# Performance work log

Hardware: AMD Instinct MI355X
Metric: run time of the kernel (lower is better)

Reference implementation:

```python
import jax, jax.numpy as jnp
import numpy as np

D_MODEL = 1024
NUM_HEADS = 16
HEAD_DIM = D_MODEL // NUM_HEADS
SEQ_LEN = 2048
THETA = 10000.0


def setup_inputs() -> dict:
    key = jax.random.key(0)
    ks = jax.random.split(key, 9)
    s = 1.0 / np.sqrt(D_MODEL)
    inp = {
        "x": jax.random.normal(ks[0], (2, SEQ_LEN, D_MODEL), dtype=jnp.float32),
        "Wq": jax.random.uniform(ks[1], (D_MODEL, D_MODEL), jnp.float32, -s, s),
        "bq": jax.random.uniform(ks[2], (D_MODEL,), jnp.float32, -s, s),
        "Wk": jax.random.uniform(ks[3], (D_MODEL, D_MODEL), jnp.float32, -s, s),
        "bk": jax.random.uniform(ks[4], (D_MODEL,), jnp.float32, -s, s),
        "Wv": jax.random.uniform(ks[5], (D_MODEL, D_MODEL), jnp.float32, -s, s),
        "bv": jax.random.uniform(ks[6], (D_MODEL,), jnp.float32, -s, s),
        "Wo": jax.random.uniform(ks[7], (D_MODEL, D_MODEL), jnp.float32, -s, s),
        "bo": jax.random.uniform(ks[8], (D_MODEL,), jnp.float32, -s, s),
    }
    return inp


def _rope_cos_sin(seq_len, dim, theta):
    inv_freq = 1.0 / theta ** (jnp.arange(0, dim, 2, dtype=jnp.float32) / dim)  # [dim/2]
    t = jnp.arange(seq_len, dtype=jnp.float32)
    freqs = jnp.outer(t, inv_freq)  # [S, dim/2]
    return jnp.cos(freqs), jnp.sin(freqs)


def _apply_rope(x, cos, sin):
    # x: [B, H, S, head_dim]; interleaved complex pairs (even, odd)
    x2 = x.reshape(*x.shape[:-1], -1, 2)  # [B,H,S,hd/2,2]
    xe, xo = x2[..., 0], x2[..., 1]
    c = cos[None, None, :, :]
    s = sin[None, None, :, :]
    oe = xe * c - xo * s
    oo = xe * s + xo * c
    return jnp.stack([oe, oo], axis=-1).reshape(x.shape)


def reference(x, Wq, bq, Wk, bk, Wv, bv, Wo, bo):
    B, S, D = x.shape
    H, hd = NUM_HEADS, HEAD_DIM
    q = x @ Wq.T + bq
    k = x @ Wk.T + bk
    v = x @ Wv.T + bv
    # [B, H, S, hd]
    q = q.reshape(B, S, H, hd).transpose(0, 2, 1, 3)
    k = k.reshape(B, S, H, hd).transpose(0, 2, 1, 3)
    v = v.reshape(B, S, H, hd).transpose(0, 2, 1, 3)
    cos, sin = _rope_cos_sin(S, hd, THETA)
    q = _apply_rope(q, cos, sin)
    k = _apply_rope(k, cos, sin)
    scores = jnp.einsum("bhqd,bhkd->bhqk", q, k) / jnp.sqrt(jnp.float32(hd))
    causal = jnp.triu(jnp.ones((S, S), dtype=bool), k=1)
    scores = jnp.where(causal[None, None, :, :], -jnp.inf, scores)
    attn = jax.nn.softmax(scores, axis=-1)
    out = jnp.einsum("bhqk,bhkd->bhqd", attn, v)
    out = out.transpose(0, 2, 1, 3).reshape(B, S, D)
    return out @ Wo.T + bo
```

## Files before the change

### kernel.cpp

```cpp
#include <hip/hip_runtime.h>
#include <hip/hip_bf16.h>

#define S_LEN 2048
#define DM 1024
#define NH 16
#define HD 64
#define M_ROWS 4096
#define LOG2E 1.4426950408889634f
#define MASKVAL -1.0e4f
#define QSCALE 0.18033688011112042f

typedef __attribute__((ext_vector_type(8))) short short8;
typedef __attribute__((ext_vector_type(2))) float f32x2;
typedef __attribute__((ext_vector_type(4))) float f32x4;
typedef __attribute__((ext_vector_type(16))) float f32x16;

__device__ inline ushort f2b(float f) {
  union { float f; unsigned u; } v; v.f = f;
  unsigned r = v.u + 0x7fffu + ((v.u >> 16) & 1u);
  return (ushort)(r >> 16);
}

__device__ inline float b2f(ushort u) {
  union { unsigned u; float f; } v; v.u = ((unsigned)u) << 16; return v.f;
}

__device__ inline unsigned pk_bf16(float a, float b) {
  __hip_bfloat162 h = __float22bfloat162_rn(make_float2(a, b));
  union { __hip_bfloat162 h; unsigned u; } v; v.h = h;
  return v.u;
}

__device__ inline float fexp2(float x) { return __builtin_amdgcn_exp2f(x); }

__device__ inline void gl_lds16(const void* g, void* l) {
  __builtin_amdgcn_global_load_lds(
      (const __attribute__((address_space(1))) void*)g,
      (__attribute__((address_space(3))) void*)l, 16, 0, 0);
}

__global__ __launch_bounds__(256) void cast_rope_kernel(
    const float* __restrict__ x, const float* __restrict__ Wq, const float* __restrict__ Wk,
    const float* __restrict__ Wv, const float* __restrict__ Wo,
    ushort* __restrict__ xb, ushort* __restrict__ Wqb, ushort* __restrict__ Wkb,
    ushort* __restrict__ Wvb, ushort* __restrict__ Wob,
    float* __restrict__ ropeC, float* __restrict__ ropeS) {
  const int bid = blockIdx.x;
  if (bid >= 8192) {
    int idx = (bid - 8192) * 256 + threadIdx.x;
    int s = idx >> 5, i = idx & 31;
    float inv = exp2f(-(float)i * (13.287712379549449f / 32.0f));
    float a = (float)s * inv;
    ropeC[idx] = cosf(a);
    ropeS[idx] = sinf(a);
    return;
  }
  int i = bid * 256 + threadIdx.x;
  int r = i >> 18, off = i & 0x3FFFF;
  const float4* s;
  uint2* d;
  switch (r) {
    case 0: case 1: case 2: case 3: s = (const float4*)x + i;  d = (uint2*)xb + i;  break;
    case 4: s = (const float4*)Wq + off; d = (uint2*)Wqb + off; break;
    case 5: s = (const float4*)Wk + off; d = (uint2*)Wkb + off; break;
    case 6: s = (const float4*)Wv + off; d = (uint2*)Wvb + off; break;
    default: s = (const float4*)Wo + off; d = (uint2*)Wob + off; break;
  }
  float4 v = *s;
  uint2 o;
  o.x = pk_bf16(v.x, v.y);
  o.y = pk_bf16(v.z, v.w);
  *d = o;
}

__global__ __launch_bounds__(256) void gemm_qkv_kernel(const ushort* __restrict__ xb,
    const ushort* __restrict__ Wqb, const ushort* __restrict__ Wkb, const ushort* __restrict__ Wvb,
    const float* __restrict__ bq, const float* __restrict__ bk, const float* __restrict__ bv,
    const float* __restrict__ ropeC, const float* __restrict__ ropeS,
    ushort* __restrict__ qb, ushort* __restrict__ kb, ushort* __restrict__ vT) {
  __shared__ ushort lds[24576];
  const int lid = blockIdx.x;
  const int swz = (lid & 7) * 96 + (lid >> 3);
  const int z = swz >> 8;
  const int rem = swz & 255;
  const int m0 = (rem & 31) * 128, n0 = (rem >> 5) * 128;
  const ushort* W = (z == 0) ? Wqb : ((z == 1) ? Wkb : Wvb);
  const float* bias = (z == 0) ? bq : ((z == 1) ? bk : bv);
  const int t = threadIdx.x, lane = t & 63, wave = t >> 6;
  const int wr = (wave >> 1) * 64, wc = (wave & 1) * 64;
  const int lr = lane & 15, lg = lane >> 4;

  const int slot0 = wave * 128 + lane, slot1 = slot0 + 64;
  const int row0 = slot0 >> 2, g0 = (slot0 & 3) ^ (row0 & 3);
  const int row1 = slot1 >> 2, g1 = (slot1 & 3) ^ (row1 & 3);
  const ushort* Ap0 = &xb[(size_t)(m0 + row0) * DM + g0 * 8];
  const ushort* Ap1 = &xb[(size_t)(m0 + row1) * DM + g1 * 8];
  const ushort* Wp0 = &W[(size_t)(n0 + row0) * DM + g0 * 8];
  const ushort* Wp1 = &W[(size_t)(n0 + row1) * DM + g1 * 8];

  f32x4 acc[4][4];
#pragma unroll
  for (int a = 0; a < 4; a++)
#pragma unroll
    for (int b = 0; b < 4; b++) acc[a][b] = (f32x4){0.f, 0.f, 0.f, 0.f};

  gl_lds16(Ap0, &lds[slot0 * 8]);
  gl_lds16(Ap1, &lds[slot1 * 8]);
  gl_lds16(Wp0, &lds[12288 + slot0 * 8]);
  gl_lds16(Wp1, &lds[12288 + slot1 * 8]);
  gl_lds16(Ap0 + 32, &lds[4096 + slot0 * 8]);
  gl_lds16(Ap1 + 32, &lds[4096 + slot1 * 8]);
  gl_lds16(Wp0 + 32, &lds[16384 + slot0 * 8]);
  gl_lds16(Wp1 + 32, &lds[16384 + slot1 * 8]);
  asm volatile("s_waitcnt vmcnt(4)" ::: "memory");
  __builtin_amdgcn_s_barrier();
  __builtin_amdgcn_sched_barrier(0);

  int cur = 0;
  for (int i = 0; i < 32; i++) {
    const bool pref = (i + 2 < 32);
    if (pref) {
      const int nb = (cur >= 1) ? cur - 1 : 2;
      const int k0 = (i + 2) * 32;
      gl_lds16(Ap0 + k0, &lds[nb * 4096 + slot0 * 8]);
      gl_lds16(Ap1 + k0, &lds[nb * 4096 + slot1 * 8]);
      gl_lds16(Wp0 + k0, &lds[12288 + nb * 4096 + slot0 * 8]);
      gl_lds16(Wp1 + k0, &lds[12288 + nb * 4096 + slot1 * 8]);
    }
    const int fb = cur * 4096;
    short8 af[4], bf[4];
#pragma unroll
    for (int mt = 0; mt < 4; mt++) {
      const int row = wr + mt * 16 + lr;
      af[mt] = *(const short8*)&lds[fb + (row * 4 + (lg ^ (row & 3))) * 8];
    }
#pragma unroll
    for (int nt = 0; nt < 4; nt++) {
      const int row = wc + nt * 16 + lr;
      bf[nt] = *(const short8*)&lds[12288 + fb + (row * 4 + (lg ^ (row & 3))) * 8];
    }
#pragma unroll
    for (int mt = 0; mt < 4; mt++)
#pragma unroll
      for (int nt = 0; nt < 4; nt++)
        acc[mt][nt] = __builtin_amdgcn_mfma_f32_16x16x32_bf16(af[mt], bf[nt], acc[mt][nt], 0, 0, 0);
    if (i + 1 < 32) {
      if (pref) asm volatile("s_waitcnt vmcnt(4)" ::: "memory");
      else      asm volatile("s_waitcnt vmcnt(0)" ::: "memory");
      __builtin_amdgcn_s_barrier();
      __builtin_amdgcn_sched_barrier(0);
    }
    cur = (cur >= 2) ? 0 : cur + 1;
  }
  __syncthreads();

#pragma unroll
  for (int mt = 0; mt < 4; mt++) {
#pragma unroll
    for (int nt = 0; nt < 4; nt++) {
      const int nloc = wc + nt * 16 + lr;
      const float bn = bias[n0 + nloc];
#pragma unroll
      for (int r = 0; r < 4; r++) {
        const int mloc = wr + mt * 16 + lg * 4 + r;
        const ushort v = f2b(acc[mt][nt][r] + bn);
        if (z < 2) lds[mloc * 136 + nloc] = v;
        else       lds[nloc * 136 + mloc] = v;
      }
    }
  }
  __syncthreads();

  const int b = m0 >> 11;
  if (z < 2) {
    ushort* dst = (z == 0) ? qb : kb;
    const float qscale = (z == 0) ? QSCALE : 1.0f;
#pragma unroll
    for (int c = 0; c < 8; c++) {
      const int sloc = c * 16 + (t >> 4);
      const int nloc = (t & 15) * 8;
      short8 val = *(const short8*)&lds[sloc * 136 + nloc];
      const int s = (m0 + sloc) & (S_LEN - 1);
      const int h = (n0 + nloc) >> 6;
      const int d0 = nloc & 63;
      const float4 cv = *(const float4*)&ropeC[s * 32 + d0 / 2];
      const float4 sv = *(const float4*)&ropeS[s * 32 + d0 / 2];
      uint4 o;
      {
        float e = b2f((ushort)val[0]), od = b2f((ushort)val[1]);
        o.x = pk_bf16((e * cv.x - od * sv.x) * qscale, (e * sv.x + od * cv.x) * qscale);
      }
      {
        float e = b2f((ushort)val[2]), od = b2f((ushort)val[3]);
        o.y = pk_bf16((e * cv.y - od * sv.y) * qscale, (e * sv.y + od * cv.y) * qscale);
      }
      {
        float e = b2f((ushort)val[4]), od = b2f((ushort)val[5]);
        o.z = pk_bf16((e * cv.z - od * sv.z) * qscale, (e * sv.z + od * cv.z) * qscale);
      }
      {
        float e = b2f((ushort)val[6]), od = b2f((ushort)val[7]);
        o.w = pk_bf16((e * cv.w - od * sv.w) * qscale, (e * sv.w + od * cv.w) * qscale);
      }
      *(uint4*)&dst[(((size_t)b * NH + h) * S_LEN + s) * HD + d0] = o;
    }
  } else {
    const int sbase = m0 & (S_LEN - 1);
#pragma unroll
    for (int c = 0; c < 8; c++) {
      const int nloc = c * 16 + (t >> 4);
      const int s0 = (t & 15) * 8;
      short8 val = *(const short8*)&lds[nloc * 136 + s0];
      const int h = (n0 + nloc) >> 6;
      const int d = nloc & 63;
      *(short8*)&vT[(((size_t)b * NH + h) * HD + d) * S_LEN + sbase + s0] = val;
    }
  }
}

__global__ __launch_bounds__(256) void flash_kernel(const ushort* __restrict__ qb,
                                                    const ushort* __restrict__ kb,
                                                    const ushort* __restrict__ vT,
                                                    ushort* __restrict__ attn) {
  __shared__ ushort lds[24576];
  const int t = threadIdx.x, lane = t & 63, wave = t >> 6;
  const int q31 = lane & 31, h = lane >> 5;
  const int lid = blockIdx.x;
  const int g = lid >> 5;
  const int qt = (g < 8) ? (15 - g) : (g - 8);
  const int bh = lid & 31;
  const int q0 = qt * 128;
  const int ntiles = 2 * qt + 2;
  const int kstart = 0;
  const int kend = ntiles;

  const ushort* kbh = kb + (size_t)bh * S_LEN * HD;
  const ushort* vbh = vT + (size_t)bh * HD * S_LEN;

  const int qrow = q0 + wave * 32 + q31;
  const ushort* qptr = qb + ((size_t)bh * S_LEN + qrow) * HD + h * 8;
  short8 qf[4];
#pragma unroll
  for (int s = 0; s < 4; s++) qf[s] = *(const short8*)(qptr + s * 16);

  const int slot0 = wave * 128 + lane, slot1 = slot0 + 64;
  const int row0 = slot0 >> 3, g0 = (slot0 & 7) ^ (row0 & 7);
  const int row1 = slot1 >> 3, g1 = (slot1 & 7) ^ (row1 & 7);
  const int lo0 = wave * 128 * 8, lo1 = lo0 + 64 * 8;

  int foff[4][2];
#pragma unroll
  for (int s = 0; s < 4; s++)
#pragma unroll
    for (int st = 0; st < 2; st++) {
      const int row = st * 32 + q31;
      foff[s][st] = (row * 8 + ((2 * s + h) ^ (row & 7))) * 8;
    }

  const ushort* kp0 = kbh + (size_t)row0 * HD + g0 * 8;
  const ushort* kp1 = kbh + (size_t)row1 * HD + g1 * 8;
  const ushort* vp0 = vbh + (size_t)row0 * S_LEN + g0 * 8;
  const ushort* vp1 = vbh + (size_t)row1 * S_LEN + g1 * 8;
  gl_lds16(kp0, &lds[lo0]);
  gl_lds16(kp1, &lds[lo1]);
  gl_lds16(vp0, &lds[12288 + lo0]);
  gl_lds16(vp1, &lds[12288 + lo1]);
  kp0 += 64 * HD; kp1 += 64 * HD; vp0 += 64; vp1 += 64;
  gl_lds16(kp0, &lds[4096 + lo0]);
  gl_lds16(kp1, &lds[4096 + lo1]);
  gl_lds16(vp0, &lds[16384 + lo0]);
  gl_lds16(vp1, &lds[16384 + lo1]);
  kp0 += 64 * HD; kp1 += 64 * HD; vp0 += 64; vp1 += 64;

  f32x16 O[2];
#pragma unroll
  for (int st = 0; st < 2; st++)
#pragma unroll
    for (int r = 0; r < 16; r++) O[st][r] = 0.f;

  f32x16 zc;
#pragma unroll
  for (int r = 0; r < 16; r++) zc[r] = 0.f;

  f32x2 lpA = (f32x2){0.f, 0.f}, lpB = (f32x2){0.f, 0.f};

  asm volatile("s_waitcnt vmcnt(4)" ::: "memory");
  __builtin_amdgcn_s_barrier();
  __builtin_amdgcn_sched_barrier(0);

  int cur = 0;
  for (int kt = kstart; kt < kend; ++kt) {
    const bool pref = (kt + 2 < kend);
    if (pref) {
      const int nb = (cur >= 1) ? cur - 1 : 2;
      const int ko = nb * 4096, vo = 12288 + nb * 4096;
      gl_lds16(kp0, &lds[ko + lo0]);
      gl_lds16(kp1, &lds[ko + lo1]);
      gl_lds16(vp0, &lds[vo + lo0]);
      gl_lds16(vp1, &lds[vo + lo1]);
      kp0 += 64 * HD; kp1 += 64 * HD; vp0 += 64; vp1 += 64;
    }
    const ushort* Kb = &lds[cur * 4096];
    const ushort* Vb = &lds[12288 + cur * 4096];

    f32x16 sc0, sc1;
    __builtin_amdgcn_s_setprio(1);
    sc0 = __builtin_amdgcn_mfma_f32_32x32x16_bf16(
        *(const short8*)&Kb[foff[0][0]], qf[0], zc, 0, 0, 0);
    sc1 = __builtin_amdgcn_mfma_f32_32x32x16_bf16(
        *(const short8*)&Kb[foff[0][1]], qf[0], zc, 0, 0, 0);
#pragma unroll
    for (int s = 1; s < 4; s++) {
      sc0 = __builtin_amdgcn_mfma_f32_32x32x16_bf16(
          *(const short8*)&Kb[foff[s][0]], qf[s], sc0, 0, 0, 0);
      sc1 = __builtin_amdgcn_mfma_f32_32x32x16_bf16(
          *(const short8*)&Kb[foff[s][1]], qf[s], sc1, 0, 0, 0);
    }
    __builtin_amdgcn_s_setprio(0);

    if (kt * 64 + 63 > q0 + wave * 32) {
#pragma unroll
      for (int r = 0; r < 16; r++) {
        const int kc0 = kt * 64 + (r & 3) + 8 * (r >> 2) + 4 * h;
        if (kc0 > qrow) sc0[r] = MASKVAL;
        if (kc0 + 32 > qrow) sc1[r] = MASKVAL;
      }
    }
#pragma unroll
    for (int r = 0; r < 16; r += 2) {
      const float a0 = fexp2(sc0[r]), a1 = fexp2(sc0[r + 1]);
      const float b0 = fexp2(sc1[r]), b1 = fexp2(sc1[r + 1]);
      sc0[r] = a0; sc0[r + 1] = a1;
      sc1[r] = b0; sc1[r + 1] = b1;
      lpA += (f32x2){a0, a1};
      lpB += (f32x2){b0, b1};
    }

    unsigned pp[8][2];
#pragma unroll
    for (int rg = 0; rg < 4; rg++) {
      pp[rg][0] = pk_bf16(sc0[4 * rg + 0], sc0[4 * rg + 1]);
      pp[rg][1] = pk_bf16(sc0[4 * rg + 2], sc0[4 * rg + 3]);
      pp[4 + rg][0] = pk_bf16(sc1[4 * rg + 0], sc1[4 * rg + 1]);
      pp[4 + rg][1] = pk_bf16(sc1[4 * rg + 2], sc1[4 * rg + 3]);
    }
    __builtin_amdgcn_s_setprio(1);
#pragma unroll
    for (int s = 0; s < 4; s++) {
      unsigned d0 = pp[2 * s][0], e0 = pp[2 * s + 1][0];
      unsigned d1 = pp[2 * s][1], e1 = pp[2 * s + 1][1];
      asm("v_permlane32_swap_b32 %0, %1" : "+v"(d0), "+v"(e0));
      asm("v_permlane32_swap_b32 %0, %1" : "+v"(d1), "+v"(e1));
      union { unsigned u[4]; short8 v; } pf;
      pf.u[0] = d0;
      pf.u[1] = d1;
      pf.u[2] = e0;
      pf.u[3] = e1;
      O[0] = __builtin_amdgcn_mfma_f32_32x32x16_bf16(
          *(const short8*)&Vb[foff[s][0]], pf.v, O[0], 0, 0, 0);
      O[1] = __builtin_amdgcn_mfma_f32_32x32x16_bf16(
          *(const short8*)&Vb[foff[s][1]], pf.v, O[1], 0, 0, 0);
    }
    __builtin_amdgcn_s_setprio(0);

    if (kt + 1 < kend) {
      if (pref) asm volatile("s_waitcnt vmcnt(4)" ::: "memory");
      else      asm volatile("s_waitcnt vmcnt(0)" ::: "memory");
      __builtin_amdgcn_s_barrier();
      __builtin_amdgcn_sched_barrier(0);
    }
    cur = (cur >= 2) ? 0 : cur + 1;
  }

  float lacc = (lpA[0] + lpA[1]) + (lpB[0] + lpB[1]);
  lacc += __shfl_xor(lacc, 32);
  const float inv = 1.f / lacc;

  const int b = bh >> 4, hh = bh & 15;
  const int q = q0 + wave * 32 + q31;
  ushort* obase = attn + ((size_t)b * S_LEN + q) * DM + hh * HD;
#pragma unroll
  for (int st = 0; st < 2; st++)
#pragma unroll
    for (int rg = 0; rg < 4; rg++) {
      const int d0 = st * 32 + 8 * rg + 4 * h;
      uint2 w;
      w.x = pk_bf16(O[st][4 * rg + 0] * inv, O[st][4 * rg + 1] * inv);
      w.y = pk_bf16(O[st][4 * rg + 2] * inv, O[st][4 * rg + 3] * inv);
      *(uint2*)&obase[d0] = w;
    }
}

__global__ __launch_bounds__(256) void gemm_out_kernel(const ushort* __restrict__ attn,
                                                       const ushort* __restrict__ Wob,
                                                       const float* __restrict__ bo,
                                                       float* __restrict__ out) {
  __shared__ ushort lds[18432];
  const int lid = blockIdx.x;
  const int swz = (lid & 7) * 64 + (lid >> 3);
  const int m0 = (swz & 31) * 128, n0 = (swz >> 5) * 64;
  const int t = threadIdx.x, lane = t & 63, wave = t >> 6;
  const int wm = (wave >> 1) * 64, wn = (wave & 1) * 32;
  const int lr = lane & 15, lg = lane >> 4;
  const int slotA0 = wave * 128 + lane, slotA1 = slotA0 + 64;
  const int rowA0 = slotA0 >> 2, gA0 = (slotA0 & 3) ^ (rowA0 & 3);
  const int rowA1 = slotA1 >> 2, gA1 = (slotA1 & 3) ^ (rowA1 & 3);
  const int slotB = wave * 64 + lane;
  const int rowB = slotB >> 2, gB = (slotB & 3) ^ (rowB & 3);
  const ushort* Ap0 = &attn[(size_t)(m0 + rowA0) * DM + gA0 * 8];
  const ushort* Ap1 = &attn[(size_t)(m0 + rowA1) * DM + gA1 * 8];
  const ushort* Wp  = &Wob[(size_t)(n0 + rowB) * DM + gB * 8];

  f32x4 acc[4][2];
#pragma unroll
  for (int a = 0; a < 4; a++)
#pragma unroll
    for (int b = 0; b < 2; b++) acc[a][b] = (f32x4){0.f, 0.f, 0.f, 0.f};

  gl_lds16(Ap0, &lds[slotA0 * 8]);
  gl_lds16(Ap1, &lds[slotA1 * 8]);
  gl_lds16(Wp, &lds[12288 + slotB * 8]);
  gl_lds16(Ap0 + 32, &lds[4096 + slotA0 * 8]);
  gl_lds16(Ap1 + 32, &lds[4096 + slotA1 * 8]);
  gl_lds16(Wp + 32, &lds[14336 + slotB * 8]);
  asm volatile("s_waitcnt vmcnt(3)" ::: "memory");
  __builtin_amdgcn_s_barrier();
  __builtin_amdgcn_sched_barrier(0);

  int cur = 0;
  for (int i = 0; i < 32; i++) {
    const bool pref = (i + 2 < 32);
    if (pref) {
      const int nb = (cur >= 1) ? cur - 1 : 2;
      const int k0 = (i + 2) * 32;
      gl_lds16(Ap0 + k0, &lds[nb * 4096 + slotA0 * 8]);
      gl_lds16(Ap1 + k0, &lds[nb * 4096 + slotA1 * 8]);
      gl_lds16(Wp + k0, &lds[12288 + nb * 2048 + slotB * 8]);
    }
    short8 af[4], bf[2];
#pragma unroll
    for (int mt = 0; mt < 4; mt++) {
      const int row = wm + mt * 16 + lr;
      af[mt] = *(const short8*)&lds[cur * 4096 + (row * 4 + (lg ^ (row & 3))) * 8];
    }
#pragma unroll
    for (int nt = 0; nt < 2; nt++) {
      const int row = wn + nt * 16 + lr;
      bf[nt] = *(const short8*)&lds[12288 + cur * 2048 + (row * 4 + (lg ^ (row & 3))) * 8];
    }
#pragma unroll
    for (int mt = 0; mt < 4; mt++)
#pragma unroll
      for (int nt = 0; nt < 2; nt++)
        acc[mt][nt] = __builtin_amdgcn_mfma_f32_16x16x32_bf16(af[mt], bf[nt], acc[mt][nt], 0, 0, 0);
    if (i + 1 < 32) {
      if (pref) asm volatile("s_waitcnt vmcnt(3)" ::: "memory");
      else      asm volatile("s_waitcnt vmcnt(0)" ::: "memory");
      __builtin_amdgcn_s_barrier();
      __builtin_amdgcn_sched_barrier(0);
    }
    cur = (cur >= 2) ? 0 : cur + 1;
  }

#pragma unroll
  for (int mt = 0; mt < 4; mt++) {
#pragma unroll
    for (int nt = 0; nt < 2; nt++) {
      const int n = n0 + wn + nt * 16 + lr;
      const float bn = bo[n];
#pragma unroll
      for (int r = 0; r < 4; r++) {
        const int m = m0 + wm + mt * 16 + lg * 4 + r;
        out[(size_t)m * DM + n] = acc[mt][nt][r] + bn;
      }
    }
  }
}

extern "C" void kernel_launch(void* const* d_in, const int* in_sizes, int n_in,
                              void* d_out, int out_size, void* d_ws, size_t ws_size,
                              hipStream_t stream) {
  const float* x  = (const float*)d_in[0];
  const float* Wq = (const float*)d_in[1];
  const float* bq = (const float*)d_in[2];
  const float* Wk = (const float*)d_in[3];
  const float* bk = (const float*)d_in[4];
  const float* Wv = (const float*)d_in[5];
  const float* bv = (const float*)d_in[6];
  const float* Wo = (const float*)d_in[7];
  const float* bo = (const float*)d_in[8];
  float* out = (float*)d_out;

  char* ws = (char*)d_ws;
  size_t off = 0;
  auto alloc = [&](size_t bytes) { char* p = ws + off; off += (bytes + 255) & ~255ull; return p; };
  ushort* xb   = (ushort*)alloc((size_t)M_ROWS * DM * 2);
  ushort* Wqb  = (ushort*)alloc((size_t)DM * DM * 2);
  ushort* Wkb  = (ushort*)alloc((size_t)DM * DM * 2);
  ushort* Wvb  = (ushort*)alloc((size_t)DM * DM * 2);
  ushort* Wob  = (ushort*)alloc((size_t)DM * DM * 2);
  ushort* qb   = (ushort*)alloc((size_t)M_ROWS * DM * 2);
  ushort* kb   = (ushort*)alloc((size_t)M_ROWS * DM * 2);
  ushort* vTb  = (ushort*)alloc((size_t)M_ROWS * DM * 2);
  ushort* attn = (ushort*)alloc((size_t)M_ROWS * DM * 2);
  float* ropeC = (float*)alloc((size_t)S_LEN * 32 * 4);
  float* ropeS = (float*)alloc((size_t)S_LEN * 32 * 4);
  (void)ws_size; (void)in_sizes; (void)n_in; (void)out_size;

  cast_rope_kernel<<<8448, 256, 0, stream>>>(x, Wq, Wk, Wv, Wo, xb, Wqb, Wkb, Wvb, Wob,
                                             ropeC, ropeS);
  gemm_qkv_kernel<<<768, 256, 0, stream>>>(
      xb, Wqb, Wkb, Wvb, bq, bk, bv, ropeC, ropeS, qb, kb, vTb);
  flash_kernel<<<512, 256, 0, stream>>>(qb, kb, vTb, attn);
  gemm_out_kernel<<<512, 256, 0, stream>>>(attn, Wob, bo, out);
}
```

Before: 188.0 us.

## Fuse all four stages into one persistent kernel with grid barriers

Replaces the four separate launches (cast/rope, QKV GEMM, flash attention, output GEMM) with a single persistent kernel of 768 blocks that runs each stage in turn, separated by software grid-wide barriers built on atomic counters in workspace. The goal is to remove launch gaps and per-kernel ramp-up and tail costs between stages. In exchange, every block must wait at each barrier for the slowest one, the flash stage's causal load imbalance is no longer absorbed by the next kernel, and 256 blocks sit idle during the last two stages. Correctness relies on all 768 blocks being resident at once (launch_bounds 256,3) and on barrier state persisting across calls via a magic-word initialisation.

```diff
diff --git a/kernel.cpp b/kernel.cpp
--- a/kernel.cpp
+++ b/kernel.cpp
@@ -10,6 +10,9 @@
 #define MASKVAL -1.0e4f
 #define QSCALE 0.18033688011112042f
 
+#define NB 768
+#define BARMAGIC 0x9E3779B1u
+
 typedef __attribute__((ext_vector_type(8))) short short8;
 typedef __attribute__((ext_vector_type(2))) float f32x2;
 typedef __attribute__((ext_vector_type(4))) float f32x4;
@@ -39,15 +42,31 @@
       (__attribute__((address_space(3))) void*)l, 16, 0, 0);
 }
 
-__global__ __launch_bounds__(256) void cast_rope_kernel(
+__device__ inline void grid_bar(unsigned* cnt, int t) {
+  __syncthreads();
+  if (t == 0) {
+    __threadfence();
+    const unsigned v = __hip_atomic_fetch_add(cnt, 1u, __ATOMIC_ACQ_REL,
+                                              __HIP_MEMORY_SCOPE_AGENT);
+    const unsigned target = (v / NB + 1u) * NB;
+    unsigned c;
+    do {
+      __builtin_amdgcn_s_sleep(4);
+      c = __hip_atomic_load(cnt, __ATOMIC_ACQUIRE, __HIP_MEMORY_SCOPE_AGENT);
+    } while (c < target);
+  }
+  __syncthreads();
+}
+
+
+__device__ inline void cast_rope_body(int vb, int t,
     const float* __restrict__ x, const float* __restrict__ Wq, const float* __restrict__ Wk,
     const float* __restrict__ Wv, const float* __restrict__ Wo,
     ushort* __restrict__ xb, ushort* __restrict__ Wqb, ushort* __restrict__ Wkb,
     ushort* __restrict__ Wvb, ushort* __restrict__ Wob,
     float* __restrict__ ropeC, float* __restrict__ ropeS) {
-  const int bid = blockIdx.x;
-  if (bid >= 8192) {
-    int idx = (bid - 8192) * 256 + threadIdx.x;
+  if (vb >= 8192) {
+    int idx = (vb - 8192) * 256 + t;
     int s = idx >> 5, i = idx & 31;
     float inv = exp2f(-(float)i * (13.287712379549449f / 32.0f));
     float a = (float)s * inv;
@@ -55,7 +74,7 @@
     ropeS[idx] = sinf(a);
     return;
   }
-  int i = bid * 256 + threadIdx.x;
+  int i = vb * 256 + t;
   int r = i >> 18, off = i & 0x3FFFF;
   const float4* s;
   uint2* d;
@@ -73,20 +92,19 @@
   *d = o;
 }
 
-__global__ __launch_bounds__(256) void gemm_qkv_kernel(const ushort* __restrict__ xb,
+__device__ void gemm_qkv_body(ushort* lds, int lid, int t,
+    const ushort* __restrict__ xb,
     const ushort* __restrict__ Wqb, const ushort* __restrict__ Wkb, const ushort* __restrict__ Wvb,
     const float* __restrict__ bq, const float* __restrict__ bk, const float* __restrict__ bv,
     const float* __restrict__ ropeC, const float* __restrict__ ropeS,
     ushort* __restrict__ qb, ushort* __restrict__ kb, ushort* __restrict__ vT) {
-  __shared__ ushort lds[24576];
-  const int lid = blockIdx.x;
   const int swz = (lid & 7) * 96 + (lid >> 3);
   const int z = swz >> 8;
   const int rem = swz & 255;
   const int m0 = (rem & 31) * 128, n0 = (rem >> 5) * 128;
   const ushort* W = (z == 0) ? Wqb : ((z == 1) ? Wkb : Wvb);
   const float* bias = (z == 0) ? bq : ((z == 1) ? bk : bv);
-  const int t = threadIdx.x, lane = t & 63, wave = t >> 6;
+  const int lane = t & 63, wave = t >> 6;
   const int wr = (wave >> 1) * 64, wc = (wave & 1) * 64;
   const int lr = lane & 15, lg = lane >> 4;
 
@@ -218,21 +236,18 @@
   }
 }
 
-__global__ __launch_bounds__(256) void flash_kernel(const ushort* __restrict__ qb,
-                                                    const ushort* __restrict__ kb,
-                                                    const ushort* __restrict__ vT,
-                                                    ushort* __restrict__ attn) {
-  __shared__ ushort lds[24576];
-  const int t = threadIdx.x, lane = t & 63, wave = t >> 6;
+__device__ void flash_body(ushort* lds, int lid, int t,
+                           const ushort* __restrict__ qb,
+                           const ushort* __restrict__ kb,
+                           const ushort* __restrict__ vT,
+                           ushort* __restrict__ attn) {
+  const int lane = t & 63, wave = t >> 6;
   const int q31 = lane & 31, h = lane >> 5;
-  const int lid = blockIdx.x;
   const int g = lid >> 5;
   const int qt = (g < 8) ? (15 - g) : (g - 8);
   const int bh = lid & 31;
   const int q0 = qt * 128;
-  const int ntiles = 2 * qt + 2;
-  const int kstart = 0;
-  const int kend = ntiles;
+  const int kend = 2 * qt + 2;
 
   const ushort* kbh = kb + (size_t)bh * S_LEN * HD;
   const ushort* vbh = vT + (size_t)bh * HD * S_LEN;
@@ -289,7 +304,7 @@
   __builtin_amdgcn_sched_barrier(0);
 
   int cur = 0;
-  for (int kt = kstart; kt < kend; ++kt) {
+  for (int kt = 0; kt < kend; ++kt) {
     const bool pref = (kt + 2 < kend);
     if (pref) {
       const int nb = (cur >= 1) ? cur - 1 : 2;
@@ -391,15 +406,14 @@
     }
 }
 
-__global__ __launch_bounds__(256) void gemm_out_kernel(const ushort* __restrict__ attn,
-                                                       const ushort* __restrict__ Wob,
-                                                       const float* __restrict__ bo,
-                                                       float* __restrict__ out) {
-  __shared__ ushort lds[18432];
-  const int lid = blockIdx.x;
+__device__ void gemm_out_body(ushort* lds, int lid, int t,
+                              const ushort* __restrict__ attn,
+                              const ushort* __restrict__ Wob,
+                              const float* __restrict__ bo,
+                              float* __restrict__ out) {
   const int swz = (lid & 7) * 64 + (lid >> 3);
   const int m0 = (swz & 31) * 128, n0 = (swz >> 5) * 64;
-  const int t = threadIdx.x, lane = t & 63, wave = t >> 6;
+  const int lane = t & 63, wave = t >> 6;
   const int wm = (wave >> 1) * 64, wn = (wave & 1) * 32;
   const int lr = lane & 15, lg = lane >> 4;
   const int slotA0 = wave * 128 + lane, slotA1 = slotA0 + 64;
@@ -475,6 +489,49 @@
       }
     }
   }
+}
+
+__global__ __launch_bounds__(256, 3) void fused_kernel(
+    const float* __restrict__ x,
+    const float* __restrict__ Wq, const float* __restrict__ bq,
+    const float* __restrict__ Wk, const float* __restrict__ bk,
+    const float* __restrict__ Wv, const float* __restrict__ bv,
+    const float* __restrict__ Wo, const float* __restrict__ bo,
+    ushort* __restrict__ xb, ushort* __restrict__ Wqb, ushort* __restrict__ Wkb,
+    ushort* __restrict__ Wvb, ushort* __restrict__ Wob,
+    ushort* __restrict__ qb, ushort* __restrict__ kb, ushort* __restrict__ vT,
+    ushort* __restrict__ attn, float* __restrict__ ropeC, float* __restrict__ ropeS,
+    float* __restrict__ out, unsigned* bars) {
+  __shared__ ushort lds[24576];
+  const int bid = blockIdx.x;
+  const int t = threadIdx.x;
+
+  if (bid == 0 && t == 0) {
+    if (__hip_atomic_load(&bars[48], __ATOMIC_ACQUIRE, __HIP_MEMORY_SCOPE_AGENT) != BARMAGIC) {
+      __hip_atomic_store(&bars[0], 0u, __ATOMIC_RELAXED, __HIP_MEMORY_SCOPE_AGENT);
+      __hip_atomic_store(&bars[16], 0u, __ATOMIC_RELAXED, __HIP_MEMORY_SCOPE_AGENT);
+      __hip_atomic_store(&bars[32], 0u, __ATOMIC_RELAXED, __HIP_MEMORY_SCOPE_AGENT);
+      __hip_atomic_store(&bars[48], BARMAGIC, __ATOMIC_RELEASE, __HIP_MEMORY_SCOPE_AGENT);
+    }
+  }
+  if (t == 0) {
+    while (__hip_atomic_load(&bars[48], __ATOMIC_ACQUIRE, __HIP_MEMORY_SCOPE_AGENT) != BARMAGIC)
+      __builtin_amdgcn_s_sleep(2);
+  }
+  __syncthreads();
+
+  for (int it = 0; it < 11; ++it)
+    cast_rope_body(bid + it * 768, t, x, Wq, Wk, Wv, Wo, xb, Wqb, Wkb, Wvb, Wob,
+                   ropeC, ropeS);
+  grid_bar(&bars[0], t);
+
+  gemm_qkv_body(lds, bid, t, xb, Wqb, Wkb, Wvb, bq, bk, bv, ropeC, ropeS, qb, kb, vT);
+  grid_bar(&bars[16], t);
+
+  if (bid < 512) flash_body(lds, bid, t, qb, kb, vT, attn);
+  grid_bar(&bars[32], t);
+
+  if (bid < 512) gemm_out_body(lds, bid, t, attn, Wob, bo, out);
 }
 
 extern "C" void kernel_launch(void* const* d_in, const int* in_sizes, int n_in,
@@ -505,12 +562,10 @@
   ushort* attn = (ushort*)alloc((size_t)M_ROWS * DM * 2);
   float* ropeC = (float*)alloc((size_t)S_LEN * 32 * 4);
   float* ropeS = (float*)alloc((size_t)S_LEN * 32 * 4);
+  unsigned* bars = (unsigned*)alloc(4096);
   (void)ws_size; (void)in_sizes; (void)n_in; (void)out_size;
 
-  cast_rope_kernel<<<8448, 256, 0, stream>>>(x, Wq, Wk, Wv, Wo, xb, Wqb, Wkb, Wvb, Wob,
-                                             ropeC, ropeS);
-  gemm_qkv_kernel<<<768, 256, 0, stream>>>(
-      xb, Wqb, Wkb, Wvb, bq, bk, bv, ropeC, ropeS, qb, kb, vTb);
-  flash_kernel<<<512, 256, 0, stream>>>(qb, kb, vTb, attn);
-  gemm_out_kernel<<<512, 256, 0, stream>>>(attn, Wob, bo, out);
-}
+  fused_kernel<<<NB, 256, 0, stream>>>(x, Wq, bq, Wk, bk, Wv, bv, Wo, bo,
+                                       xb, Wqb, Wkb, Wvb, Wob, qb, kb, vTb, attn,
+                                       ropeC, ropeS, out, bars);
+}
```

Result: slower. 533.6 us (+183.8%).
